# Kernel optimization log

Measured on AMD Instinct MI355X. Metric: run time of the kernel, lower is better.

Reference implementation:

```python
import jax, jax.numpy as jnp
import numpy as np

B, L, C, D, K = 32, 36864, 16, 512, 24


def setup_inputs() -> dict:
    key = jax.random.key(0)
    ks = jax.random.split(key, 5)
    x = jax.random.normal(ks[0], (B, L, C), jnp.float32)
    # offset-conv weights scaled small so predicted offsets are O(0.2) (kaiming-ish but tame)
    w_off = jax.random.normal(ks[1], (2 * K, C, K), jnp.float32) * 0.01
    b_off = jax.random.normal(ks[2], (2 * K,), jnp.float32) * 0.05
    w_def = jax.random.normal(ks[3], (D, C, K), jnp.float32) * (2.0 / (C * K)) ** 0.5
    b_def = jax.random.normal(ks[4], (D,), jnp.float32) * 0.05
    return {"x": x, "w_off": w_off, "b_off": b_off, "w_def": w_def, "b_def": b_def}


def reference(x, w_off, b_off, w_def, b_def):
    # x: [B, L, C] -> torch view [B, C, 1, L]; H == 1 throughout.
    Bn, Ln, Cn = x.shape
    twoK, _, Kn = w_off.shape
    Lout = Ln // Kn
    xc = jnp.transpose(x, (0, 2, 1))                 # [B, C, L]
    xk = xc.reshape(Bn, Cn, Lout, Kn)                # stride == kernel -> non-overlapping windows
    # offset conv: [B, 2K, Lout]
    off = jnp.einsum('bclk,ock->bol', xk, w_off) + b_off[None, :, None]
    off = off.reshape(Bn, Kn, 2, Lout)               # channel 2k -> dy, 2k+1 -> dx (torchvision layout)
    dy = jnp.transpose(off[:, :, 0, :], (0, 2, 1))   # [B, Lout, K]
    dx = jnp.transpose(off[:, :, 1, :], (0, 2, 1))   # [B, Lout, K]
    # sampling positions along width; base = w_out*K + k
    base = jnp.arange(Lout * Kn, dtype=x.dtype).reshape(Lout, Kn)
    px = base[None] + dx                             # [B, Lout, K]
    # height bilinear weight: with H=1, contribution at h=0 is max(0, 1-|dy|)
    wy = jnp.maximum(jnp.array(0, x.dtype), 1.0 - jnp.abs(dy))
    # width bilinear with zero padding (torchvision bilinear_interpolate semantics)
    valid = (px > -1.0) & (px < Ln)
    x0 = jnp.floor(px)
    lw = px - x0                                     # weight for right neighbor
    i0 = x0.astype(jnp.int32)
    i1 = i0 + 1
    m0 = (valid & (i0 >= 0) & (i0 < Ln)).astype(x.dtype)
    m1 = (valid & (i1 >= 0) & (i1 < Ln)).astype(x.dtype)
    i0c = jnp.broadcast_to(jnp.clip(i0, 0, Ln - 1).reshape(Bn, 1, Lout * Kn), (Bn, Cn, Lout * Kn))
    i1c = jnp.broadcast_to(jnp.clip(i1, 0, Ln - 1).reshape(Bn, 1, Lout * Kn), (Bn, Cn, Lout * Kn))
    v0 = jnp.take_along_axis(xc, i0c, axis=2).reshape(Bn, Cn, Lout, Kn)
    v1 = jnp.take_along_axis(xc, i1c, axis=2).reshape(Bn, Cn, Lout, Kn)
    val = (v0 * ((1.0 - lw) * m0)[:, None] + v1 * (lw * m1)[:, None]) * wy[:, None]  # [B,C,Lout,K]
    out = jnp.einsum('bclk,dck->bld', val, w_def) + b_def  # [B, Lout, D]
    return out
```

## Files before the change

### kernel.cpp

```cpp
#include <hip/hip_runtime.h>
#include <stdint.h>

#define BATCH 32
#define LLEN  36864
#define CCH   16
#define DOUT  512
#define KW    24
#define LOUT  1536
#define MROWS (BATCH * LOUT)
#define CK    384
#define TWOK  48
#define NMK   (MROWS * KW)

typedef float fx4 __attribute__((ext_vector_type(4)));
typedef float f32x4 __attribute__((ext_vector_type(4)));
typedef __bf16 bf16x8 __attribute__((ext_vector_type(8)));
typedef uint32_t u32x4 __attribute__((ext_vector_type(4)));

__device__ __forceinline__ void gload16(void* lds, const void* g)
{
    __builtin_amdgcn_global_load_lds(
        (const __attribute__((address_space(1))) uint32_t*)g,
        (__attribute__((address_space(3))) uint32_t*)lds, 16, 0, 0);
}

__global__ __launch_bounds__(256) void prep_kernel(
    const float* __restrict__ w_off, const float* __restrict__ w_def,
    __bf16* __restrict__ woff_b, __bf16* __restrict__ wdef_b)
{
    int idx = blockIdx.x * 256 + threadIdx.x;
    if (idx < TWOK * CK) {
        int o = idx / CK, rem = idx % CK;
        int k = rem >> 4, c = rem & 15;
        woff_b[idx] = (__bf16)w_off[o * CK + c * KW + k];
    }
    if (idx < DOUT * CK) {
        int d = idx / CK, rem = idx % CK;
        int k = rem >> 4, c = rem & 15;
        wdef_b[idx] = (__bf16)w_def[d * CK + c * KW + k];
    }
}

__global__ __launch_bounds__(256, 3) void offsets_kernel(
    const float* __restrict__ x, const __bf16* __restrict__ woff_b,
    const float* __restrict__ b_off, uint32_t* __restrict__ dxy)
{
    __shared__ __bf16 Bs[TWOK * 392];
    __shared__ float  offS[64 * 49];

    const int t = threadIdx.x;
#pragma unroll
    for (int i = 0; i < 9; ++i) {
        int ch = t + 256 * i;
        int row = ch / 48, cc = ch % 48;
        *(u32x4*)&Bs[row * 392 + cc * 8] =
            *(const u32x4*)&woff_b[row * CK + cc * 8];
    }
    __syncthreads();

    const int wave = t >> 6, lane = t & 63;
    const int quad = lane >> 4, l16 = lane & 15;
    const int m0 = blockIdx.x * 64;
    const int row = m0 + wave * 16 + l16;
    const float* xr = x + (size_t)row * CK;

    f32x4 acc[3] = {};
#pragma unroll
    for (int ks = 0; ks < 12; ++ks) {
        int k0 = ks * 32 + quad * 8;
        fx4 a0 = *(const fx4*)&xr[k0];
        fx4 a1 = *(const fx4*)&xr[k0 + 4];
        bf16x8 af;
        af[0] = (__bf16)a0.x; af[1] = (__bf16)a0.y;
        af[2] = (__bf16)a0.z; af[3] = (__bf16)a0.w;
        af[4] = (__bf16)a1.x; af[5] = (__bf16)a1.y;
        af[6] = (__bf16)a1.z; af[7] = (__bf16)a1.w;
#pragma unroll
        for (int j = 0; j < 3; ++j) {
            bf16x8 bf = *(const bf16x8*)&Bs[(j * 16 + l16) * 392 + k0];
            acc[j] = __builtin_amdgcn_mfma_f32_16x16x32_bf16(af, bf, acc[j], 0, 0, 0);
        }
    }
#pragma unroll
    for (int j = 0; j < 3; ++j)
#pragma unroll
        for (int r = 0; r < 4; ++r)
            offS[(wave * 16 + quad * 4 + r) * 49 + j * 16 + l16] = acc[j][r];
    __syncthreads();

#pragma unroll
    for (int s = 0; s < 6; ++s) {
        int id = t + 256 * s;
        int r = id / 24, k = id - r * 24;
        float dy = offS[r * 49 + 2 * k]     + b_off[2 * k];
        float dx = offS[r * 49 + 2 * k + 1] + b_off[2 * k + 1];
        union { __bf16 h[2]; uint32_t u; } p;
        p.h[0] = (__bf16)dy; p.h[1] = (__bf16)dx;
        dxy[(size_t)m0 * KW + id] = p.u;
    }
}

__global__ __launch_bounds__(256) void gather_kernel(
    const float* __restrict__ x, const uint32_t* __restrict__ dxy,
    __bf16* __restrict__ val)
{
    int id = blockIdx.x * 256 + threadIdx.x;
    int b = id / (LOUT * KW);
    int pos = id - b * (LOUT * KW);

    union { uint32_t u; __bf16 h[2]; } p;
    p.u = dxy[id];
    float dy = (float)p.h[0], dx = (float)p.h[1];

    float wy  = fmaxf(0.f, 1.f - fabsf(dy));
    float px  = (float)pos + dx;
    float x0f = floorf(px);
    float lw  = px - x0f;
    int   i0  = (int)x0f;
    bool valid = (px > -1.0f) && (px < (float)LLEN);
    float w0 = (valid && i0 >= 0)         ? (1.f - lw) * wy : 0.f;
    float w1 = (valid && (i0 + 1) < LLEN) ? lw * wy         : 0.f;
    int i0c = min(max(i0, 0), LLEN - 1);
    int i1c = min(max(i0 + 1, 0), LLEN - 1);

    const float* xb = x + (size_t)b * LLEN * CCH;
    const fx4* p0 = (const fx4*)&xb[(size_t)i0c * CCH];
    const fx4* p1 = (const fx4*)&xb[(size_t)i1c * CCH];

    bf16x8 o0, o1;
#pragma unroll
    for (int q = 0; q < 2; ++q) {
        fx4 v0 = p0[q], v1 = p1[q];
        o0[q * 4 + 0] = (__bf16)(w0 * v0.x + w1 * v1.x);
        o0[q * 4 + 1] = (__bf16)(w0 * v0.y + w1 * v1.y);
        o0[q * 4 + 2] = (__bf16)(w0 * v0.z + w1 * v1.z);
        o0[q * 4 + 3] = (__bf16)(w0 * v0.w + w1 * v1.w);
    }
#pragma unroll
    for (int q = 0; q < 2; ++q) {
        fx4 v0 = p0[q + 2], v1 = p1[q + 2];
        o1[q * 4 + 0] = (__bf16)(w0 * v0.x + w1 * v1.x);
        o1[q * 4 + 1] = (__bf16)(w0 * v0.y + w1 * v1.y);
        o1[q * 4 + 2] = (__bf16)(w0 * v0.z + w1 * v1.z);
        o1[q * 4 + 3] = (__bf16)(w0 * v0.w + w1 * v1.w);
    }
    __bf16* vp = val + (size_t)id * 16;
    *(bf16x8*)vp       = o0;
    *(bf16x8*)(vp + 8) = o1;
}

#define BM 128
#define BN 256
#define BK 64

__global__ __launch_bounds__(512, 4) void gemm_kernel(
    const __bf16* __restrict__ A, const __bf16* __restrict__ Bw,
    const float* __restrict__ bias, float* __restrict__ out)
{
    __shared__ __bf16 As[BM * BK];
    __shared__ __bf16 Bs[BN * BK];

    const int t = threadIdx.x;
    const int m0 = blockIdx.x * BM;
    const int n0 = blockIdx.y * BN;
    const int wave = t >> 6, lane = t & 63;
    const int quad = lane >> 4, l16 = lane & 15;
    const int wr = wave >> 2, wc = wave & 3;

    f32x4 acc[4][4] = {};
    const __bf16* Ag = A + (size_t)m0 * CK;
    const __bf16* Bg = Bw + (size_t)n0 * CK;

    for (int kt = 0; kt < CK; kt += BK) {
        __syncthreads();
#pragma unroll
        for (int it = 0; it < 2; ++it) {
            int q = it * 512 + t;
            int r = q >> 3, c8 = q & 7;
            int sc = c8 ^ (r & 7);
            gload16(&As[q * 8], Ag + (size_t)r * CK + kt + sc * 8);
        }
#pragma unroll
        for (int it = 0; it < 4; ++it) {
            int q = it * 512 + t;
            int r = q >> 3, c8 = q & 7;
            int sc = c8 ^ (r & 7);
            gload16(&Bs[q * 8], Bg + (size_t)r * CK + kt + sc * 8);
        }
        __syncthreads();
#pragma unroll
        for (int ks = 0; ks < 2; ++ks) {
            bf16x8 af[4], bfr[4];
#pragma unroll
            for (int i = 0; i < 4; ++i) {
                int row = wr * 64 + i * 16 + l16;
                af[i] = *(const bf16x8*)&As[row * BK + (((ks * 4 + quad) ^ (row & 7)) * 8)];
                int col = wc * 64 + i * 16 + l16;
                bfr[i] = *(const bf16x8*)&Bs[col * BK + (((ks * 4 + quad) ^ (col & 7)) * 8)];
            }
#pragma unroll
            for (int i = 0; i < 4; ++i)
#pragma unroll
                for (int j = 0; j < 4; ++j)
                    acc[i][j] = __builtin_amdgcn_mfma_f32_16x16x32_bf16(
                        af[i], bfr[j], acc[i][j], 0, 0, 0);
        }
    }

#pragma unroll
    for (int j = 0; j < 4; ++j) {
        int col = n0 + wc * 64 + j * 16 + l16;
        float bj = bias[col];
#pragma unroll
        for (int i = 0; i < 4; ++i) {
            int rowb = m0 + wr * 64 + i * 16 + quad * 4;
#pragma unroll
            for (int r = 0; r < 4; ++r)
                out[(size_t)(rowb + r) * DOUT + col] = acc[i][j][r] + bj;
        }
    }
}

extern "C" void kernel_launch(void* const* d_in, const int* in_sizes, int n_in,
                              void* d_out, int out_size, void* d_ws, size_t ws_size,
                              hipStream_t stream)
{
    const float* x     = (const float*)d_in[0];
    const float* w_off = (const float*)d_in[1];
    const float* b_off = (const float*)d_in[2];
    const float* w_def = (const float*)d_in[3];
    const float* b_def = (const float*)d_in[4];
    float* out = (float*)d_out;

    char* ws = (char*)d_ws;
    __bf16*   val    = (__bf16*)ws;
    __bf16*   wdef_b = (__bf16*)(ws + 37748736);
    __bf16*   woff_b = (__bf16*)(ws + 38141952);
    uint32_t* dxy    = (uint32_t*)(ws + 38178816);

    prep_kernel<<<768, 256, 0, stream>>>(w_off, w_def, woff_b, wdef_b);
    offsets_kernel<<<MROWS / 64, 256, 0, stream>>>(x, woff_b, b_off, dxy);
    gather_kernel<<<NMK / 256, 256, 0, stream>>>(x, dxy, val);
    gemm_kernel<<<dim3(MROWS / BM, DOUT / BN), 512, 0, stream>>>(val, wdef_b, b_def, out);
}
```

Before: 226.2 us.

## Fuse bilinear gather into GEMM A-tile production, dropping val buffer

Removes the separate gather kernel and its bf16 intermediate. The GEMM now computes the bilinear-sampled A tile in registers from x and the packed offsets, and writes it straight into LDS. The next k-slice's gather loads are prefetched during the MFMA loop. The GEMM tile shrinks to 64x256 with 256 threads. This costs redundant gather work across the two N blocks and more B-tile traffic per output row.

```diff
diff --git a/kernel.cpp b/kernel.cpp
--- a/kernel.cpp
+++ b/kernel.cpp
@@ -10,7 +10,6 @@
 #define MROWS (BATCH * LOUT)
 #define CK    384
 #define TWOK  48
-#define NMK   (MROWS * KW)
 
 typedef float fx4 __attribute__((ext_vector_type(4)));
 typedef float f32x4 __attribute__((ext_vector_type(4)));
@@ -100,62 +99,14 @@
     }
 }
 
-__global__ __launch_bounds__(256) void gather_kernel(
-    const float* __restrict__ x, const uint32_t* __restrict__ dxy,
-    __bf16* __restrict__ val)
-{
-    int id = blockIdx.x * 256 + threadIdx.x;
-    int b = id / (LOUT * KW);
-    int pos = id - b * (LOUT * KW);
-
-    union { uint32_t u; __bf16 h[2]; } p;
-    p.u = dxy[id];
-    float dy = (float)p.h[0], dx = (float)p.h[1];
-
-    float wy  = fmaxf(0.f, 1.f - fabsf(dy));
-    float px  = (float)pos + dx;
-    float x0f = floorf(px);
-    float lw  = px - x0f;
-    int   i0  = (int)x0f;
-    bool valid = (px > -1.0f) && (px < (float)LLEN);
-    float w0 = (valid && i0 >= 0)         ? (1.f - lw) * wy : 0.f;
-    float w1 = (valid && (i0 + 1) < LLEN) ? lw * wy         : 0.f;
-    int i0c = min(max(i0, 0), LLEN - 1);
-    int i1c = min(max(i0 + 1, 0), LLEN - 1);
-
-    const float* xb = x + (size_t)b * LLEN * CCH;
-    const fx4* p0 = (const fx4*)&xb[(size_t)i0c * CCH];
-    const fx4* p1 = (const fx4*)&xb[(size_t)i1c * CCH];
-
-    bf16x8 o0, o1;
-#pragma unroll
-    for (int q = 0; q < 2; ++q) {
-        fx4 v0 = p0[q], v1 = p1[q];
-        o0[q * 4 + 0] = (__bf16)(w0 * v0.x + w1 * v1.x);
-        o0[q * 4 + 1] = (__bf16)(w0 * v0.y + w1 * v1.y);
-        o0[q * 4 + 2] = (__bf16)(w0 * v0.z + w1 * v1.z);
-        o0[q * 4 + 3] = (__bf16)(w0 * v0.w + w1 * v1.w);
-    }
-#pragma unroll
-    for (int q = 0; q < 2; ++q) {
-        fx4 v0 = p0[q + 2], v1 = p1[q + 2];
-        o1[q * 4 + 0] = (__bf16)(w0 * v0.x + w1 * v1.x);
-        o1[q * 4 + 1] = (__bf16)(w0 * v0.y + w1 * v1.y);
-        o1[q * 4 + 2] = (__bf16)(w0 * v0.z + w1 * v1.z);
-        o1[q * 4 + 3] = (__bf16)(w0 * v0.w + w1 * v1.w);
-    }
-    __bf16* vp = val + (size_t)id * 16;
-    *(bf16x8*)vp       = o0;
-    *(bf16x8*)(vp + 8) = o1;
-}
-
-#define BM 128
+#define BM 64
 #define BN 256
 #define BK 64
 
-__global__ __launch_bounds__(512, 4) void gemm_kernel(
-    const __bf16* __restrict__ A, const __bf16* __restrict__ Bw,
-    const float* __restrict__ bias, float* __restrict__ out)
+__global__ __launch_bounds__(256) void gemm_fused(
+    const float* __restrict__ x, const uint32_t* __restrict__ dxy,
+    const __bf16* __restrict__ Bw, const float* __restrict__ bias,
+    float* __restrict__ out)
 {
     __shared__ __bf16 As[BM * BK];
     __shared__ __bf16 Bs[BN * BK];
@@ -165,37 +116,80 @@
     const int n0 = blockIdx.y * BN;
     const int wave = t >> 6, lane = t & 63;
     const int quad = lane >> 4, l16 = lane & 15;
-    const int wr = wave >> 2, wc = wave & 3;
+
+    const int mloc = t >> 2, k4 = t & 3;
+    const int Mrow = m0 + mloc;
+    const int b    = Mrow / LOUT;
+    const int lb   = Mrow - b * LOUT;
+    const float* xb = x + (size_t)b * LLEN * CCH;
 
     f32x4 acc[4][4] = {};
-    const __bf16* Ag = A + (size_t)m0 * CK;
     const __bf16* Bg = Bw + (size_t)n0 * CK;
+
+    fx4 g0[4], g1[4];
+    float w0, w1;
+
+    auto load_pair = [&](int kk) {
+        union { uint32_t u; __bf16 h[2]; } p;
+        p.u = dxy[(size_t)Mrow * KW + kk];
+        float dy = (float)p.h[0], dx = (float)p.h[1];
+        float wy  = fmaxf(0.f, 1.f - fabsf(dy));
+        float px  = (float)(lb * KW + kk) + dx;
+        float x0f = floorf(px);
+        float lw  = px - x0f;
+        int   i0  = (int)x0f;
+        bool valid = (px > -1.0f) && (px < (float)LLEN);
+        w0 = (valid && i0 >= 0)         ? (1.f - lw) * wy : 0.f;
+        w1 = (valid && (i0 + 1) < LLEN) ? lw * wy         : 0.f;
+        int i0c = min(max(i0, 0), LLEN - 1);
+        int i1c = min(max(i0 + 1, 0), LLEN - 1);
+        const fx4* p0 = (const fx4*)&xb[(size_t)i0c * CCH];
+        const fx4* p1 = (const fx4*)&xb[(size_t)i1c * CCH];
+#pragma unroll
+        for (int q = 0; q < 4; ++q) { g0[q] = p0[q]; g1[q] = p1[q]; }
+    };
+
+    load_pair(k4);
 
     for (int kt = 0; kt < CK; kt += BK) {
         __syncthreads();
-#pragma unroll
-        for (int it = 0; it < 2; ++it) {
-            int q = it * 512 + t;
-            int r = q >> 3, c8 = q & 7;
-            int sc = c8 ^ (r & 7);
-            gload16(&As[q * 8], Ag + (size_t)r * CK + kt + sc * 8);
-        }
-#pragma unroll
-        for (int it = 0; it < 4; ++it) {
-            int q = it * 512 + t;
+        bf16x8 oa, ob;
+#pragma unroll
+        for (int q = 0; q < 2; ++q) {
+            fx4 v0 = g0[q], v1 = g1[q];
+            oa[q * 4 + 0] = (__bf16)(w0 * v0.x + w1 * v1.x);
+            oa[q * 4 + 1] = (__bf16)(w0 * v0.y + w1 * v1.y);
+            oa[q * 4 + 2] = (__bf16)(w0 * v0.z + w1 * v1.z);
+            oa[q * 4 + 3] = (__bf16)(w0 * v0.w + w1 * v1.w);
+        }
+#pragma unroll
+        for (int q = 0; q < 2; ++q) {
+            fx4 v0 = g0[q + 2], v1 = g1[q + 2];
+            ob[q * 4 + 0] = (__bf16)(w0 * v0.x + w1 * v1.x);
+            ob[q * 4 + 1] = (__bf16)(w0 * v0.y + w1 * v1.y);
+            ob[q * 4 + 2] = (__bf16)(w0 * v0.z + w1 * v1.z);
+            ob[q * 4 + 3] = (__bf16)(w0 * v0.w + w1 * v1.w);
+        }
+        int g = 2 * k4;
+        *(bf16x8*)&As[mloc * BK + ((g ^ (mloc & 7)) * 8)]       = oa;
+        *(bf16x8*)&As[mloc * BK + (((g + 1) ^ (mloc & 7)) * 8)] = ob;
+#pragma unroll
+        for (int it = 0; it < 8; ++it) {
+            int q = it * 256 + t;
             int r = q >> 3, c8 = q & 7;
             int sc = c8 ^ (r & 7);
             gload16(&Bs[q * 8], Bg + (size_t)r * CK + kt + sc * 8);
         }
         __syncthreads();
+        if (kt + BK < CK) load_pair((kt >> 4) + 4 + k4);
 #pragma unroll
         for (int ks = 0; ks < 2; ++ks) {
             bf16x8 af[4], bfr[4];
 #pragma unroll
             for (int i = 0; i < 4; ++i) {
-                int row = wr * 64 + i * 16 + l16;
+                int row = i * 16 + l16;
                 af[i] = *(const bf16x8*)&As[row * BK + (((ks * 4 + quad) ^ (row & 7)) * 8)];
-                int col = wc * 64 + i * 16 + l16;
+                int col = wave * 64 + i * 16 + l16;
                 bfr[i] = *(const bf16x8*)&Bs[col * BK + (((ks * 4 + quad) ^ (col & 7)) * 8)];
             }
 #pragma unroll
@@ -209,11 +203,11 @@
 
 #pragma unroll
     for (int j = 0; j < 4; ++j) {
-        int col = n0 + wc * 64 + j * 16 + l16;
+        int col = n0 + wave * 64 + j * 16 + l16;
         float bj = bias[col];
 #pragma unroll
         for (int i = 0; i < 4; ++i) {
-            int rowb = m0 + wr * 64 + i * 16 + quad * 4;
+            int rowb = m0 + i * 16 + quad * 4;
 #pragma unroll
             for (int r = 0; r < 4; ++r)
                 out[(size_t)(rowb + r) * DOUT + col] = acc[i][j][r] + bj;
@@ -233,13 +227,11 @@
     float* out = (float*)d_out;
 
     char* ws = (char*)d_ws;
-    __bf16*   val    = (__bf16*)ws;
-    __bf16*   wdef_b = (__bf16*)(ws + 37748736);
-    __bf16*   woff_b = (__bf16*)(ws + 38141952);
-    uint32_t* dxy    = (uint32_t*)(ws + 38178816);
+    uint32_t* dxy    = (uint32_t*)ws;
+    __bf16*   wdef_b = (__bf16*)(ws + 4718592);
+    __bf16*   woff_b = (__bf16*)(ws + 5111808);
 
     prep_kernel<<<768, 256, 0, stream>>>(w_off, w_def, woff_b, wdef_b);
     offsets_kernel<<<MROWS / 64, 256, 0, stream>>>(x, woff_b, b_off, dxy);
-    gather_kernel<<<NMK / 256, 256, 0, stream>>>(x, dxy, val);
-    gemm_kernel<<<dim3(MROWS / BM, DOUT / BN), 512, 0, stream>>>(val, wdef_b, b_def, out);
-}
+    gemm_fused<<<dim3(MROWS / BM, DOUT / BN), 256, 0, stream>>>(x, dxy, wdef_b, b_def, out);
+}
```

Measured after the change: 212.2 us. -6.2%, faster.
